# Performance work log

Hardware: AMD Instinct MI355X
Metric: run time of the kernel (lower is better)

## Reference

```python
import jax, jax.numpy as jnp
import numpy as np

NEG_SLOPE = 0.2

def gat_conv(x, src, dst, n_nodes, W, a_src, a_dst, bias, heads, out_ch, concat):
    # Linear transform per head: (N, H, C)
    h = (x @ W).reshape(n_nodes, heads, out_ch)
    # Per-node attention logits (N, H)
    al_src = jnp.sum(h * a_src, axis=-1)
    al_dst = jnp.sum(h * a_dst, axis=-1)
    # Per-edge score with LeakyReLU (E, H)
    e = jax.nn.leaky_relu(al_src[src] + al_dst[dst], NEG_SLOPE)
    # Segment softmax over incoming edges of each dst node
    m = jax.ops.segment_max(e, dst, num_segments=n_nodes)
    e = jnp.exp(e - jax.lax.stop_gradient(m)[dst])
    denom = jax.ops.segment_sum(e, dst, num_segments=n_nodes)
    alpha = e / denom[dst]                      # (E, H)
    # Weighted scatter-aggregate of source features
    msg = h[src] * alpha[:, :, None]            # (E, H, C)
    out = jax.ops.segment_sum(msg, dst, num_segments=n_nodes)  # (N, H, C)
    out = out.reshape(n_nodes, heads * out_ch) if concat else out.mean(axis=1)
    return out + bias


def setup_inputs() -> dict:
    key = jax.random.key(0)
    ks = jax.random.split(key, 12)
    N, E = 100000, 1600000
    IN, HID, OUT, H1 = 256, 128, 4, 2
    x = jax.random.normal(ks[0], (N, IN), dtype=jnp.float32)
    edge_index = jax.random.randint(ks[1], (2, E), 0, N, dtype=jnp.int64)
    s = 1.0 / np.sqrt(IN)
    W1 = jax.random.uniform(ks[2], (IN, H1 * HID), jnp.float32, -s, s)
    a_src1 = jax.random.uniform(ks[3], (H1, HID), jnp.float32, -s, s)
    a_dst1 = jax.random.uniform(ks[4], (H1, HID), jnp.float32, -s, s)
    b1 = jnp.zeros((H1 * HID,), jnp.float32)
    s2 = 1.0 / np.sqrt(H1 * HID)
    W2 = jax.random.uniform(ks[5], (H1 * HID, OUT), jnp.float32, -s2, s2)
    a_src2 = jax.random.uniform(ks[6], (1, OUT), jnp.float32, -s2, s2)
    a_dst2 = jax.random.uniform(ks[7], (1, OUT), jnp.float32, -s2, s2)
    b2 = jnp.zeros((OUT,), jnp.float32)
    return {"x": x, "edge_index": edge_index, "W1": W1, "a_src1": a_src1,
            "a_dst1": a_dst1, "b1": b1, "W2": W2, "a_src2": a_src2,
            "a_dst2": a_dst2, "b2": b2}


def reference(x, edge_index, W1, a_src1, a_dst1, b1, W2, a_src2, a_dst2, b2):
    N = x.shape[0]
    # PyG GATConv default: add self-loops
    loop = jnp.arange(N, dtype=edge_index.dtype)
    src = jnp.concatenate([edge_index[0], loop])
    dst = jnp.concatenate([edge_index[1], loop])
    h = gat_conv(x, src, dst, N, W1, a_src1, a_dst1, b1, heads=2, out_ch=128, concat=True)
    h = jax.nn.relu(h)
    # dropout p=0.4 skipped (eval mode)
    out = gat_conv(h, src, dst, N, W2, a_src2, a_dst2, b2, heads=1, out_ch=4, concat=False)
    return jax.nn.log_softmax(out, axis=1)
```

## Files before the change

kernel.cpp:

```cpp
#include <hip/hip_runtime.h>
#include <hip/hip_bf16.h>

#define NEG_SLOPE 0.2f
#define SCAN_TPB 256
#define SCAN_VPT 4
#define SCAN_ELEMS (SCAN_TPB * SCAN_VPT)

typedef __attribute__((ext_vector_type(8))) short short8;
typedef __attribute__((ext_vector_type(4))) float f32x4;

static __device__ __forceinline__ unsigned short f2bf(float v) {
    __hip_bfloat16 b = __float2bfloat16(v);
    return *reinterpret_cast<unsigned short*>(&b);
}
static __device__ __forceinline__ float bf2f(unsigned short u) {
    unsigned int x = ((unsigned int)u) << 16;
    return __uint_as_float(x);
}
static __device__ __forceinline__ float lrelu(float v) {
    return (v > 0.f) ? v : NEG_SLOPE * v;
}


__global__ void hist_kernel(const int* __restrict__ dst_idx, int* __restrict__ count,
                            int E, int N) {
    int e = blockIdx.x * blockDim.x + threadIdx.x;
    int EN = E + N;
    if (e >= EN) return;
    int d = (e < E) ? dst_idx[e] : (e - E);
    atomicAdd(&count[d], 1);
}

__global__ void scan_blocks_kernel(const int* __restrict__ count, int* __restrict__ local_ex,
                                   int* __restrict__ blockSums, int n) {
    __shared__ int sm[SCAN_TPB];
    int tid = threadIdx.x;
    int base = blockIdx.x * SCAN_ELEMS + tid * SCAN_VPT;
    int v[SCAN_VPT];
    int s = 0;
#pragma unroll
    for (int i = 0; i < SCAN_VPT; i++) {
        v[i] = (base + i < n) ? count[base + i] : 0;
        s += v[i];
    }
    sm[tid] = s;
    __syncthreads();
#pragma unroll
    for (int off = 1; off < SCAN_TPB; off <<= 1) {
        int t = (tid >= off) ? sm[tid - off] : 0;
        __syncthreads();
        sm[tid] += t;
        __syncthreads();
    }
    int ex = sm[tid] - s;
#pragma unroll
    for (int i = 0; i < SCAN_VPT; i++) {
        if (base + i < n) local_ex[base + i] = ex;
        ex += v[i];
    }
    if (tid == SCAN_TPB - 1) blockSums[blockIdx.x] = sm[tid];
}

__global__ void scan_sums_kernel(int* __restrict__ blockSums, int nb) {
    __shared__ int sm[128];
    int tid = threadIdx.x;
    int v = (tid < nb) ? blockSums[tid] : 0;
    sm[tid] = v;
    __syncthreads();
    for (int off = 1; off < 128; off <<= 1) {
        int t = (tid >= off) ? sm[tid - off] : 0;
        __syncthreads();
        sm[tid] += t;
        __syncthreads();
    }
    if (tid < nb) blockSums[tid] = sm[tid] - v;
}

__global__ void scan_finalize_kernel(int* __restrict__ offsets, const int* __restrict__ blockSums,
                                     int* __restrict__ cursor, int n, int total) {
    int tid = threadIdx.x;
    int base = blockIdx.x * SCAN_ELEMS + tid * SCAN_VPT;
    int add = blockSums[blockIdx.x];
#pragma unroll
    for (int i = 0; i < SCAN_VPT; i++) {
        int idx = base + i;
        if (idx < n) {
            int val = offsets[idx] + add;
            offsets[idx] = val;
            cursor[idx] = val;
        }
    }
    if (blockIdx.x == 0 && tid == 0) offsets[n] = total;
}

__global__ void scatter_kernel(const int* __restrict__ src_idx, const int* __restrict__ dst_idx,
                               int* __restrict__ cursor, int* __restrict__ csr_src,
                               int E, int N) {
    int e = blockIdx.x * blockDim.x + threadIdx.x;
    int EN = E + N;
    if (e >= EN) return;
    int s, d;
    if (e < E) {
        s = src_idx[e];
        d = dst_idx[e];
    } else {
        s = d = e - E;
    }
    int pos = atomicAdd(&cursor[d], 1);
    csr_src[pos] = s;
}


__global__ __launch_bounds__(256) void prep_w1t(const float* __restrict__ W1,
                                                unsigned short* __restrict__ W1t) {
    __shared__ float tile[32][33];
    int bx = blockIdx.x & 7;
    int by = blockIdx.x >> 3;
    int tx = threadIdx.x & 31;
    int ty = threadIdx.x >> 5;
#pragma unroll
    for (int i = 0; i < 4; i++) {
        int k = by * 32 + ty + i * 8;
        tile[ty + i * 8][tx] = W1[k * 256 + bx * 32 + tx];
    }
    __syncthreads();
#pragma unroll
    for (int i = 0; i < 4; i++) {
        int c = bx * 32 + ty + i * 8;
        W1t[(size_t)c * 256 + by * 32 + tx] = f2bf(tile[tx][ty + i * 8]);
    }
}


__global__ __launch_bounds__(256) void gemm1_kernel(
    const float* __restrict__ x, const unsigned short* __restrict__ W1t,
    const float* __restrict__ a_src1, const float* __restrict__ a_dst1,
    unsigned short* __restrict__ h1, float* __restrict__ al_src1,
    float* __restrict__ al_dst1, int N) {
    const int tid = threadIdx.x;
    const int w = tid >> 6, l = tid & 63;
    const int lc = l & 15, lg = l >> 4;

    const int arow = blockIdx.x * 64 + w * 16 + lc;
    const int arowc = (arow < N) ? arow : (N - 1);

    f32x4 acc[16];
#pragma unroll
    for (int j = 0; j < 16; j++) acc[j] = (f32x4){0.f, 0.f, 0.f, 0.f};

    const float* xp = x + (size_t)arowc * 256 + lg * 8;

    for (int k0 = 0; k0 < 256; k0 += 32) {
        float4 v0 = *reinterpret_cast<const float4*>(xp + k0);
        float4 v1 = *reinterpret_cast<const float4*>(xp + k0 + 4);
        short8 af;
        af[0] = (short)f2bf(v0.x);
        af[1] = (short)f2bf(v0.y);
        af[2] = (short)f2bf(v0.z);
        af[3] = (short)f2bf(v0.w);
        af[4] = (short)f2bf(v1.x);
        af[5] = (short)f2bf(v1.y);
        af[6] = (short)f2bf(v1.z);
        af[7] = (short)f2bf(v1.w);
        const unsigned short* wp = W1t + (size_t)lc * 256 + k0 + lg * 8;
#pragma unroll
        for (int j = 0; j < 16; j++) {
            short8 bf = *reinterpret_cast<const short8*>(wp + (size_t)j * 16 * 256);
            acc[j] = __builtin_amdgcn_mfma_f32_16x16x32_bf16(af, bf, acc[j], 0, 0, 0);
        }
    }

    const int rbase = blockIdx.x * 64 + w * 16 + lg * 4;

#pragma unroll
    for (int j = 0; j < 16; j++) {
#pragma unroll
        for (int r = 0; r < 4; r++) {
            int rr = rbase + r;
            if (rr < N) h1[(size_t)rr * 256 + j * 16 + lc] = f2bf(acc[j][r]);
        }
    }

    float as_[16], ad_[16];
#pragma unroll
    for (int j = 0; j < 16; j++) {
        as_[j] = a_src1[j * 16 + lc];
        ad_[j] = a_dst1[j * 16 + lc];
    }
#pragma unroll
    for (int r = 0; r < 4; r++) {
        float s0 = 0.f, d0 = 0.f, s1 = 0.f, d1 = 0.f;
#pragma unroll
        for (int j = 0; j < 8; j++) {
            s0 += acc[j][r] * as_[j];
            d0 += acc[j][r] * ad_[j];
        }
#pragma unroll
        for (int j = 8; j < 16; j++) {
            s1 += acc[j][r] * as_[j];
            d1 += acc[j][r] * ad_[j];
        }
#pragma unroll
        for (int mask = 8; mask >= 1; mask >>= 1) {
            s0 += __shfl_xor(s0, mask, 64);
            s1 += __shfl_xor(s1, mask, 64);
            d0 += __shfl_xor(d0, mask, 64);
            d1 += __shfl_xor(d1, mask, 64);
        }
        int rr = rbase + r;
        if (lc == 0 && rr < N) {
            al_src1[rr * 2 + 0] = s0;
            al_src1[rr * 2 + 1] = s1;
            al_dst1[rr * 2 + 0] = d0;
            al_dst1[rr * 2 + 1] = d1;
        }
    }
}


__global__ __launch_bounds__(256) void agg1_kernel(
    const unsigned short* __restrict__ h1,
    const float* __restrict__ al_src1, const float* __restrict__ al_dst1,
    const int* __restrict__ offsets, const int* __restrict__ csr_src,
    const float* __restrict__ b1, const float* __restrict__ W2,
    const float* __restrict__ a_src2, const float* __restrict__ a_dst2,
    float* __restrict__ g2out, float* __restrict__ al_src2o,
    float* __restrict__ al_dst2o, int N) {
    int wid = (blockIdx.x * blockDim.x + threadIdx.x) >> 6;
    if (wid >= N) return;
    int lane = threadIdx.x & 63;
    int head = lane >> 5;
    int ch = lane * 4;

    int beg = offsets[wid], end = offsets[wid + 1];
    float aldv = al_dst1[wid * 2 + head];

    float l = 0.f, p0 = 0.f, p1 = 0.f, p2 = 0.f, p3 = 0.f;

    int e = beg;
    for (; e + 3 < end; e += 4) {
        int sa = csr_src[e];
        int sb = csr_src[e + 1];
        int sc = csr_src[e + 2];
        int sd = csr_src[e + 3];
        float la = al_src1[sa * 2 + head] + aldv;
        float lb = al_src1[sb * 2 + head] + aldv;
        float lcv = al_src1[sc * 2 + head] + aldv;
        float ld = al_src1[sd * 2 + head] + aldv;
        ushort4 ha = *reinterpret_cast<const ushort4*>(h1 + (size_t)sa * 256 + ch);
        ushort4 hb = *reinterpret_cast<const ushort4*>(h1 + (size_t)sb * 256 + ch);
        ushort4 hc = *reinterpret_cast<const ushort4*>(h1 + (size_t)sc * 256 + ch);
        ushort4 hd = *reinterpret_cast<const ushort4*>(h1 + (size_t)sd * 256 + ch);
        float wa = __expf(lrelu(la));
        float wb = __expf(lrelu(lb));
        float wc = __expf(lrelu(lcv));
        float wd = __expf(lrelu(ld));
        p0 += wa * bf2f(ha.x) + wb * bf2f(hb.x) + wc * bf2f(hc.x) + wd * bf2f(hd.x);
        p1 += wa * bf2f(ha.y) + wb * bf2f(hb.y) + wc * bf2f(hc.y) + wd * bf2f(hd.y);
        p2 += wa * bf2f(ha.z) + wb * bf2f(hb.z) + wc * bf2f(hc.z) + wd * bf2f(hd.z);
        p3 += wa * bf2f(ha.w) + wb * bf2f(hb.w) + wc * bf2f(hc.w) + wd * bf2f(hd.w);
        l += (wa + wb) + (wc + wd);
    }
    for (; e < end; ++e) {
        int sa = csr_src[e];
        float la = al_src1[sa * 2 + head] + aldv;
        ushort4 ha = *reinterpret_cast<const ushort4*>(h1 + (size_t)sa * 256 + ch);
        float wa = __expf(lrelu(la));
        p0 += wa * bf2f(ha.x);
        p1 += wa * bf2f(ha.y);
        p2 += wa * bf2f(ha.z);
        p3 += wa * bf2f(ha.w);
        l += wa;
    }

    float inv = 1.f / l;
    float4 bb = *reinterpret_cast<const float4*>(b1 + ch);
    float r0 = fmaxf(p0 * inv + bb.x, 0.f);
    float r1 = fmaxf(p1 * inv + bb.y, 0.f);
    float r2 = fmaxf(p2 * inv + bb.z, 0.f);
    float r3 = fmaxf(p3 * inv + bb.w, 0.f);

    float4 w0 = *reinterpret_cast<const float4*>(W2 + (size_t)(ch + 0) * 4);
    float4 w1 = *reinterpret_cast<const float4*>(W2 + (size_t)(ch + 1) * 4);
    float4 w2 = *reinterpret_cast<const float4*>(W2 + (size_t)(ch + 2) * 4);
    float4 w3 = *reinterpret_cast<const float4*>(W2 + (size_t)(ch + 3) * 4);
    float g0 = r0 * w0.x + r1 * w1.x + r2 * w2.x + r3 * w3.x;
    float g1 = r0 * w0.y + r1 * w1.y + r2 * w2.y + r3 * w3.y;
    float g2v = r0 * w0.z + r1 * w1.z + r2 * w2.z + r3 * w3.z;
    float g3 = r0 * w0.w + r1 * w1.w + r2 * w2.w + r3 * w3.w;
#pragma unroll
    for (int mask = 32; mask >= 1; mask >>= 1) {
        g0 += __shfl_xor(g0, mask, 64);
        g1 += __shfl_xor(g1, mask, 64);
        g2v += __shfl_xor(g2v, mask, 64);
        g3 += __shfl_xor(g3, mask, 64);
    }
    if (lane == 0) {
        float4 gv;
        gv.x = g0; gv.y = g1; gv.z = g2v; gv.w = g3;
        *reinterpret_cast<float4*>(g2out + (size_t)wid * 4) = gv;
        al_src2o[wid] = g0 * a_src2[0] + g1 * a_src2[1] + g2v * a_src2[2] + g3 * a_src2[3];
        al_dst2o[wid] = g0 * a_dst2[0] + g1 * a_dst2[1] + g2v * a_dst2[2] + g3 * a_dst2[3];
    }
}


__global__ __launch_bounds__(256) void agg2_kernel(
    const float* __restrict__ g2, const float* __restrict__ al_src2,
    const float* __restrict__ al_dst2, const int* __restrict__ offsets,
    const int* __restrict__ csr_src, const float* __restrict__ b2,
    float* __restrict__ out, int N) {
    int wid = (blockIdx.x * blockDim.x + threadIdx.x) >> 6;
    if (wid >= N) return;
    int lane = threadIdx.x & 63;

    int beg = offsets[wid], end = offsets[wid + 1];
    float aldv = al_dst2[wid];

    float l = 0.f, p0 = 0.f, p1 = 0.f, p2 = 0.f, p3 = 0.f;

    int e = beg;
    for (; e + 3 < end; e += 4) {
        int sa = csr_src[e];
        int sb = csr_src[e + 1];
        int sc = csr_src[e + 2];
        int sd = csr_src[e + 3];
        float la = al_src2[sa] + aldv;
        float lb = al_src2[sb] + aldv;
        float lcv = al_src2[sc] + aldv;
        float ld = al_src2[sd] + aldv;
        float4 ga = *reinterpret_cast<const float4*>(g2 + (size_t)sa * 4);
        float4 gb = *reinterpret_cast<const float4*>(g2 + (size_t)sb * 4);
        float4 gc = *reinterpret_cast<const float4*>(g2 + (size_t)sc * 4);
        float4 gd = *reinterpret_cast<const float4*>(g2 + (size_t)sd * 4);
        float wa = __expf(lrelu(la));
        float wb = __expf(lrelu(lb));
        float wc = __expf(lrelu(lcv));
        float wd = __expf(lrelu(ld));
        p0 += wa * ga.x + wb * gb.x + wc * gc.x + wd * gd.x;
        p1 += wa * ga.y + wb * gb.y + wc * gc.y + wd * gd.y;
        p2 += wa * ga.z + wb * gb.z + wc * gc.z + wd * gd.z;
        p3 += wa * ga.w + wb * gb.w + wc * gc.w + wd * gd.w;
        l += (wa + wb) + (wc + wd);
    }
    for (; e < end; ++e) {
        int sa = csr_src[e];
        float la = al_src2[sa] + aldv;
        float4 ga = *reinterpret_cast<const float4*>(g2 + (size_t)sa * 4);
        float wa = __expf(lrelu(la));
        p0 += wa * ga.x;
        p1 += wa * ga.y;
        p2 += wa * ga.z;
        p3 += wa * ga.w;
        l += wa;
    }

    float inv = 1.f / l;
    float r0 = p0 * inv + b2[0];
    float r1 = p1 * inv + b2[1];
    float r2 = p2 * inv + b2[2];
    float r3 = p3 * inv + b2[3];
    float mx = fmaxf(fmaxf(r0, r1), fmaxf(r2, r3));
    float s0 = __expf(r0 - mx), s1 = __expf(r1 - mx), s2 = __expf(r2 - mx), s3 = __expf(r3 - mx);
    float ls = __logf(s0 + s1 + s2 + s3);
    if (lane == 0) {
        float4 ov;
        ov.x = r0 - mx - ls;
        ov.y = r1 - mx - ls;
        ov.z = r2 - mx - ls;
        ov.w = r3 - mx - ls;
        *reinterpret_cast<float4*>(out + (size_t)wid * 4) = ov;
    }
}


extern "C" void kernel_launch(void* const* d_in, const int* in_sizes, int n_in,
                              void* d_out, int out_size, void* d_ws, size_t ws_size,
                              hipStream_t stream) {
    const float* x = (const float*)d_in[0];
    const int* edge_index = (const int*)d_in[1];
    const float* W1 = (const float*)d_in[2];
    const float* a_src1 = (const float*)d_in[3];
    const float* a_dst1 = (const float*)d_in[4];
    const float* b1 = (const float*)d_in[5];
    const float* W2 = (const float*)d_in[6];
    const float* a_src2 = (const float*)d_in[7];
    const float* a_dst2 = (const float*)d_in[8];
    const float* b2 = (const float*)d_in[9];
    float* out = (float*)d_out;

    const int N = in_sizes[0] / 256;
    const int E = in_sizes[1] / 2;
    const int EN = E + N;
    const int* src_idx = edge_index;
    const int* dst_idx = edge_index + E;

    char* ws = (char*)d_ws;
    size_t off = 0;
    auto alloc = [&](size_t bytes) -> char* {
        char* p = ws + off;
        off += (bytes + 255) & ~(size_t)255;
        return p;
    };
    unsigned short* h1 = (unsigned short*)alloc((size_t)N * 256 * 2);
    unsigned short* W1t = (unsigned short*)alloc((size_t)256 * 256 * 2);
    float* al_src1 = (float*)alloc((size_t)N * 2 * 4);
    float* al_dst1 = (float*)alloc((size_t)N * 2 * 4);
    float* g2 = (float*)alloc((size_t)N * 4 * 4);
    float* al_src2 = (float*)alloc((size_t)N * 4);
    float* al_dst2 = (float*)alloc((size_t)N * 4);
    int* offsets = (int*)alloc((size_t)(N + 1) * 4);
    int* cursor = (int*)alloc((size_t)N * 4);
    int* csr_src = (int*)alloc((size_t)EN * 4);
    int* blockSums = (int*)alloc(128 * 4);

    hipMemsetAsync(cursor, 0, (size_t)N * 4, stream);

    prep_w1t<<<64, 256, 0, stream>>>(W1, W1t);

    int hb = (EN + 255) / 256;
    hist_kernel<<<hb, 256, 0, stream>>>(dst_idx, cursor, E, N);

    int nb = (N + SCAN_ELEMS - 1) / SCAN_ELEMS;
    scan_blocks_kernel<<<nb, SCAN_TPB, 0, stream>>>(cursor, offsets, blockSums, N);
    scan_sums_kernel<<<1, 128, 0, stream>>>(blockSums, nb);
    scan_finalize_kernel<<<nb, SCAN_TPB, 0, stream>>>(offsets, blockSums, cursor, N, EN);

    scatter_kernel<<<hb, 256, 0, stream>>>(src_idx, dst_idx, cursor, csr_src, E, N);

    int gb = (N + 63) / 64;
    gemm1_kernel<<<gb, 256, 0, stream>>>(x, W1t, a_src1, a_dst1, h1, al_src1, al_dst1, N);

    int ab = (N + 3) / 4;
    agg1_kernel<<<ab, 256, 0, stream>>>(h1, al_src1, al_dst1, offsets, csr_src, b1, W2,
                                        a_src2, a_dst2, g2, al_src2, al_dst2, N);
    agg2_kernel<<<ab, 256, 0, stream>>>(g2, al_src2, al_dst2, offsets, csr_src, b2, out, N);
}
```

Before: 682.9 us.

## Stage pre-swizzled W1 tiles through double-buffered LDS in gemm1

W1 is now pre-converted to bf16 in a swizzled layout that matches the MFMA B-fragment order. gemm1 cooperatively loads each 32-wide K-slice into a double-buffered shared-memory tile instead of having every wave read B fragments straight from global memory. The x row fragments are also loaded and converted to bf16 up front, all at once. The aim is to cut redundant global/L2 traffic for W1 across the four waves and to overlap loading the next slice with the current MFMAs. The cost is extra barriers per K step, 32KB of LDS per block, and more registers, which could reduce occupancy.

```diff
diff --git a/kernel.cpp b/kernel.cpp
--- a/kernel.cpp
+++ b/kernel.cpp
@@ -111,32 +111,23 @@
 }
 
 
-__global__ __launch_bounds__(256) void prep_w1t(const float* __restrict__ W1,
-                                                unsigned short* __restrict__ W1t) {
-    __shared__ float tile[32][33];
-    int bx = blockIdx.x & 7;
-    int by = blockIdx.x >> 3;
-    int tx = threadIdx.x & 31;
-    int ty = threadIdx.x >> 5;
-#pragma unroll
-    for (int i = 0; i < 4; i++) {
-        int k = by * 32 + ty + i * 8;
-        tile[ty + i * 8][tx] = W1[k * 256 + bx * 32 + tx];
-    }
-    __syncthreads();
-#pragma unroll
-    for (int i = 0; i < 4; i++) {
-        int c = bx * 32 + ty + i * 8;
-        W1t[(size_t)c * 256 + by * 32 + tx] = f2bf(tile[tx][ty + i * 8]);
-    }
+__global__ __launch_bounds__(256) void prep_w1s(const float* __restrict__ W1,
+                                                unsigned short* __restrict__ W1s) {
+    int idx = blockIdx.x * 256 + threadIdx.x;
+    int col = idx & 255;
+    int k = idx >> 8;
+    int t = k >> 5, lg = (k >> 3) & 3, kk = k & 7;
+    W1s[t * 8192 + lg * 2048 + col * 8 + kk] = f2bf(W1[k * 256 + col]);
 }
 
 
 __global__ __launch_bounds__(256) void gemm1_kernel(
-    const float* __restrict__ x, const unsigned short* __restrict__ W1t,
+    const float* __restrict__ x, const unsigned short* __restrict__ W1s,
     const float* __restrict__ a_src1, const float* __restrict__ a_dst1,
     unsigned short* __restrict__ h1, float* __restrict__ al_src1,
     float* __restrict__ al_dst1, int N) {
+    __shared__ unsigned short smB[2][8192];
+
     const int tid = threadIdx.x;
     const int w = tid >> 6, l = tid & 63;
     const int lc = l & 15, lg = l >> 4;
@@ -144,31 +135,69 @@
     const int arow = blockIdx.x * 64 + w * 16 + lc;
     const int arowc = (arow < N) ? arow : (N - 1);
 
+    const float* xp = x + (size_t)arowc * 256 + lg * 8;
+    short8 af[8];
+#pragma unroll
+    for (int t = 0; t < 8; t++) {
+        float4 v0 = *reinterpret_cast<const float4*>(xp + t * 32);
+        float4 v1 = *reinterpret_cast<const float4*>(xp + t * 32 + 4);
+        af[t][0] = (short)f2bf(v0.x);
+        af[t][1] = (short)f2bf(v0.y);
+        af[t][2] = (short)f2bf(v0.z);
+        af[t][3] = (short)f2bf(v0.w);
+        af[t][4] = (short)f2bf(v1.x);
+        af[t][5] = (short)f2bf(v1.y);
+        af[t][6] = (short)f2bf(v1.z);
+        af[t][7] = (short)f2bf(v1.w);
+    }
+
     f32x4 acc[16];
 #pragma unroll
     for (int j = 0; j < 16; j++) acc[j] = (f32x4){0.f, 0.f, 0.f, 0.f};
 
-    const float* xp = x + (size_t)arowc * 256 + lg * 8;
-
-    for (int k0 = 0; k0 < 256; k0 += 32) {
-        float4 v0 = *reinterpret_cast<const float4*>(xp + k0);
-        float4 v1 = *reinterpret_cast<const float4*>(xp + k0 + 4);
-        short8 af;
-        af[0] = (short)f2bf(v0.x);
-        af[1] = (short)f2bf(v0.y);
-        af[2] = (short)f2bf(v0.z);
-        af[3] = (short)f2bf(v0.w);
-        af[4] = (short)f2bf(v1.x);
-        af[5] = (short)f2bf(v1.y);
-        af[6] = (short)f2bf(v1.z);
-        af[7] = (short)f2bf(v1.w);
-        const unsigned short* wp = W1t + (size_t)lc * 256 + k0 + lg * 8;
+    uint4 st[4];
+    const uint4* gws = reinterpret_cast<const uint4*>(W1s);
+
+#define STAGE_LOAD(t)                         \
+    {                                         \
+        const uint4* gs = gws + (t) * 1024;   \
+        st[0] = gs[tid];                      \
+        st[1] = gs[tid + 256];                \
+        st[2] = gs[tid + 512];                \
+        st[3] = gs[tid + 768];                \
+    }
+#define STAGE_WRITE(buf)                                   \
+    {                                                      \
+        uint4* ls = reinterpret_cast<uint4*>(smB[(buf)]);  \
+        ls[tid] = st[0];                                   \
+        ls[tid + 256] = st[1];                             \
+        ls[tid + 512] = st[2];                             \
+        ls[tid + 768] = st[3];                             \
+    }
+
+    STAGE_LOAD(0)
+    STAGE_WRITE(0)
+    STAGE_LOAD(1)
+    __syncthreads();
+
+    const unsigned short* bpbase;
+#pragma unroll
+    for (int t = 0; t < 8; t++) {
+        bpbase = smB[t & 1] + lg * 2048 + lc * 8;
 #pragma unroll
         for (int j = 0; j < 16; j++) {
-            short8 bf = *reinterpret_cast<const short8*>(wp + (size_t)j * 16 * 256);
-            acc[j] = __builtin_amdgcn_mfma_f32_16x16x32_bf16(af, bf, acc[j], 0, 0, 0);
-        }
-    }
+            short8 bf = *reinterpret_cast<const short8*>(bpbase + j * 128);
+            acc[j] = __builtin_amdgcn_mfma_f32_16x16x32_bf16(af[t], bf, acc[j], 0, 0, 0);
+        }
+        if (t + 1 < 8) {
+            __syncthreads();
+            STAGE_WRITE((t + 1) & 1)
+            if (t + 2 < 8) STAGE_LOAD(t + 2)
+            __syncthreads();
+        }
+    }
+#undef STAGE_LOAD
+#undef STAGE_WRITE
 
     const int rbase = blockIdx.x * 64 + w * 16 + lg * 4;
 
@@ -403,7 +432,7 @@
         return p;
     };
     unsigned short* h1 = (unsigned short*)alloc((size_t)N * 256 * 2);
-    unsigned short* W1t = (unsigned short*)alloc((size_t)256 * 256 * 2);
+    unsigned short* W1s = (unsigned short*)alloc((size_t)256 * 256 * 2);
     float* al_src1 = (float*)alloc((size_t)N * 2 * 4);
     float* al_dst1 = (float*)alloc((size_t)N * 2 * 4);
     float* g2 = (float*)alloc((size_t)N * 4 * 4);
@@ -416,7 +445,7 @@
 
     hipMemsetAsync(cursor, 0, (size_t)N * 4, stream);
 
-    prep_w1t<<<64, 256, 0, stream>>>(W1, W1t);
+    prep_w1s<<<256, 256, 0, stream>>>(W1, W1s);
 
     int hb = (EN + 255) / 256;
     hist_kernel<<<hb, 256, 0, stream>>>(dst_idx, cursor, E, N);
@@ -429,7 +458,7 @@
     scatter_kernel<<<hb, 256, 0, stream>>>(src_idx, dst_idx, cursor, csr_src, E, N);
 
     int gb = (N + 63) / 64;
-    gemm1_kernel<<<gb, 256, 0, stream>>>(x, W1t, a_src1, a_dst1, h1, al_src1, al_dst1, N);
+    gemm1_kernel<<<gb, 256, 0, stream>>>(x, W1s, a_src1, a_dst1, h1, al_src1, al_dst1, N);
 
     int ab = (N + 3) / 4;
     agg1_kernel<<<ab, 256, 0, stream>>>(h1, al_src1, al_dst1, offsets, csr_src, b1, W2,
```

After: 663.4 us. -2.9%, faster.

## Pre-convert x to bf16, swizzle W1 layout, and map agg2 one node per thread

Applied to the files above, without the earlier changes.

Adds a separate kernel that converts x to bf16 ahead of time, and rearranges W1 into a swizzled layout so each lane's MFMA B fragments are contiguous. gemm1 now loads all A fragments up front and gets launch-bounds occupancy hints. agg2 previously ran one whole wavefront per node doing redundant work; it now processes one node per thread. The cost is an extra pass writing x as bf16 plus a larger workspace.

```diff
diff --git a/kernel.cpp b/kernel.cpp
--- a/kernel.cpp
+++ b/kernel.cpp
@@ -111,29 +111,33 @@
 }
 
 
-__global__ __launch_bounds__(256) void prep_w1t(const float* __restrict__ W1,
-                                                unsigned short* __restrict__ W1t) {
-    __shared__ float tile[32][33];
-    int bx = blockIdx.x & 7;
-    int by = blockIdx.x >> 3;
-    int tx = threadIdx.x & 31;
-    int ty = threadIdx.x >> 5;
-#pragma unroll
-    for (int i = 0; i < 4; i++) {
-        int k = by * 32 + ty + i * 8;
-        tile[ty + i * 8][tx] = W1[k * 256 + bx * 32 + tx];
-    }
-    __syncthreads();
-#pragma unroll
-    for (int i = 0; i < 4; i++) {
-        int c = bx * 32 + ty + i * 8;
-        W1t[(size_t)c * 256 + by * 32 + tx] = f2bf(tile[tx][ty + i * 8]);
-    }
-}
-
-
-__global__ __launch_bounds__(256) void gemm1_kernel(
-    const float* __restrict__ x, const unsigned short* __restrict__ W1t,
+__global__ __launch_bounds__(256) void prep_xs(const float* __restrict__ x,
+                                               unsigned short* __restrict__ xs, int total8) {
+    int i = blockIdx.x * 256 + threadIdx.x;
+    if (i >= total8) return;
+    float4 v0 = *reinterpret_cast<const float4*>(x + (size_t)i * 8);
+    float4 v1 = *reinterpret_cast<const float4*>(x + (size_t)i * 8 + 4);
+    ushort4 u0, u1;
+    u0.x = f2bf(v0.x); u0.y = f2bf(v0.y); u0.z = f2bf(v0.z); u0.w = f2bf(v0.w);
+    u1.x = f2bf(v1.x); u1.y = f2bf(v1.y); u1.z = f2bf(v1.z); u1.w = f2bf(v1.w);
+    *reinterpret_cast<ushort4*>(xs + (size_t)i * 8) = u0;
+    *reinterpret_cast<ushort4*>(xs + (size_t)i * 8 + 4) = u1;
+}
+
+
+__global__ __launch_bounds__(256) void prep_w1s(const float* __restrict__ W1,
+                                                unsigned short* __restrict__ W1s) {
+    int idx = blockIdx.x * 256 + threadIdx.x;
+    int col = idx & 255;
+    int k = idx >> 8;
+    int t = k >> 5, lg = (k >> 3) & 3, kk = k & 7;
+    int j = col >> 4, lc = col & 15;
+    W1s[t * 8192 + lg * 2048 + lc * 128 + j * 8 + kk] = f2bf(W1[k * 256 + col]);
+}
+
+
+__global__ __launch_bounds__(256, 4) void gemm1_kernel(
+    const unsigned short* __restrict__ xs, const unsigned short* __restrict__ W1s,
     const float* __restrict__ a_src1, const float* __restrict__ a_dst1,
     unsigned short* __restrict__ h1, float* __restrict__ al_src1,
     float* __restrict__ al_dst1, int N) {
@@ -144,29 +148,23 @@
     const int arow = blockIdx.x * 64 + w * 16 + lc;
     const int arowc = (arow < N) ? arow : (N - 1);
 
+    const unsigned short* xp = xs + (size_t)arowc * 256 + lg * 8;
+    short8 af[8];
+#pragma unroll
+    for (int t = 0; t < 8; t++) af[t] = *reinterpret_cast<const short8*>(xp + t * 32);
+
     f32x4 acc[16];
 #pragma unroll
     for (int j = 0; j < 16; j++) acc[j] = (f32x4){0.f, 0.f, 0.f, 0.f};
 
-    const float* xp = x + (size_t)arowc * 256 + lg * 8;
-
-    for (int k0 = 0; k0 < 256; k0 += 32) {
-        float4 v0 = *reinterpret_cast<const float4*>(xp + k0);
-        float4 v1 = *reinterpret_cast<const float4*>(xp + k0 + 4);
-        short8 af;
-        af[0] = (short)f2bf(v0.x);
-        af[1] = (short)f2bf(v0.y);
-        af[2] = (short)f2bf(v0.z);
-        af[3] = (short)f2bf(v0.w);
-        af[4] = (short)f2bf(v1.x);
-        af[5] = (short)f2bf(v1.y);
-        af[6] = (short)f2bf(v1.z);
-        af[7] = (short)f2bf(v1.w);
-        const unsigned short* wp = W1t + (size_t)lc * 256 + k0 + lg * 8;
+    const unsigned short* wbase = W1s + lg * 2048 + lc * 128;
+#pragma unroll
+    for (int t = 0; t < 8; t++) {
+        const unsigned short* wp = wbase + t * 8192;
 #pragma unroll
         for (int j = 0; j < 16; j++) {
-            short8 bf = *reinterpret_cast<const short8*>(wp + (size_t)j * 16 * 256);
-            acc[j] = __builtin_amdgcn_mfma_f32_16x16x32_bf16(af, bf, acc[j], 0, 0, 0);
+            short8 bf = *reinterpret_cast<const short8*>(wp + j * 8);
+            acc[j] = __builtin_amdgcn_mfma_f32_16x16x32_bf16(af[t], bf, acc[j], 0, 0, 0);
         }
     }
 
@@ -310,12 +308,11 @@
     const float* __restrict__ al_dst2, const int* __restrict__ offsets,
     const int* __restrict__ csr_src, const float* __restrict__ b2,
     float* __restrict__ out, int N) {
-    int wid = (blockIdx.x * blockDim.x + threadIdx.x) >> 6;
-    if (wid >= N) return;
-    int lane = threadIdx.x & 63;
-
-    int beg = offsets[wid], end = offsets[wid + 1];
-    float aldv = al_dst2[wid];
+    int nid = blockIdx.x * 256 + threadIdx.x;
+    if (nid >= N) return;
+
+    int beg = offsets[nid], end = offsets[nid + 1];
+    float aldv = al_dst2[nid];
 
     float l = 0.f, p0 = 0.f, p1 = 0.f, p2 = 0.f, p3 = 0.f;
 
@@ -363,14 +360,12 @@
     float mx = fmaxf(fmaxf(r0, r1), fmaxf(r2, r3));
     float s0 = __expf(r0 - mx), s1 = __expf(r1 - mx), s2 = __expf(r2 - mx), s3 = __expf(r3 - mx);
     float ls = __logf(s0 + s1 + s2 + s3);
-    if (lane == 0) {
-        float4 ov;
-        ov.x = r0 - mx - ls;
-        ov.y = r1 - mx - ls;
-        ov.z = r2 - mx - ls;
-        ov.w = r3 - mx - ls;
-        *reinterpret_cast<float4*>(out + (size_t)wid * 4) = ov;
-    }
+    float4 ov;
+    ov.x = r0 - mx - ls;
+    ov.y = r1 - mx - ls;
+    ov.z = r2 - mx - ls;
+    ov.w = r3 - mx - ls;
+    *reinterpret_cast<float4*>(out + (size_t)nid * 4) = ov;
 }
 
 
@@ -403,7 +398,8 @@
         return p;
     };
     unsigned short* h1 = (unsigned short*)alloc((size_t)N * 256 * 2);
-    unsigned short* W1t = (unsigned short*)alloc((size_t)256 * 256 * 2);
+    unsigned short* xs = (unsigned short*)alloc((size_t)N * 256 * 2);
+    unsigned short* W1s = (unsigned short*)alloc((size_t)256 * 256 * 2);
     float* al_src1 = (float*)alloc((size_t)N * 2 * 4);
     float* al_dst1 = (float*)alloc((size_t)N * 2 * 4);
     float* g2 = (float*)alloc((size_t)N * 4 * 4);
@@ -416,7 +412,9 @@
 
     hipMemsetAsync(cursor, 0, (size_t)N * 4, stream);
 
-    prep_w1t<<<64, 256, 0, stream>>>(W1, W1t);
+    prep_w1s<<<256, 256, 0, stream>>>(W1, W1s);
+    int total8 = N * 32;
+    prep_xs<<<(total8 + 255) / 256, 256, 0, stream>>>(x, xs, total8);
 
     int hb = (EN + 255) / 256;
     hist_kernel<<<hb, 256, 0, stream>>>(dst_idx, cursor, E, N);
@@ -429,10 +427,11 @@
     scatter_kernel<<<hb, 256, 0, stream>>>(src_idx, dst_idx, cursor, csr_src, E, N);
 
     int gb = (N + 63) / 64;
-    gemm1_kernel<<<gb, 256, 0, stream>>>(x, W1t, a_src1, a_dst1, h1, al_src1, al_dst1, N);
+    gemm1_kernel<<<gb, 256, 0, stream>>>(xs, W1s, a_src1, a_dst1, h1, al_src1, al_dst1, N);
 
     int ab = (N + 3) / 4;
     agg1_kernel<<<ab, 256, 0, stream>>>(h1, al_src1, al_dst1, offsets, csr_src, b1, W2,
                                         a_src2, a_dst2, g2, al_src2, al_dst2, N);
-    agg2_kernel<<<ab, 256, 0, stream>>>(g2, al_src2, al_dst2, offsets, csr_src, b2, out, N);
-}
+    agg2_kernel<<<(N + 255) / 256, 256, 0, stream>>>(g2, al_src2, al_dst2, offsets, csr_src,
+                                                     b2, out, N);
+}
```

Result: faster. 627.2 us (-8.2%).
